# Optimization experiments

Measured on AMD Instinct MI355X. Metric: run time of the kernel, lower is better.

## Reference

```python
import jax, jax.numpy as jnp
import numpy as np

E, T, D, H = 8, 2048, 1024, 4096  # experts, tokens/expert, n_embed, n_mlp_hidden


def setup_inputs() -> dict:
    key = jax.random.key(0)
    ks = jax.random.split(key, 4)
    return {
        "x": jax.random.normal(ks[0], (E, T, D), dtype=jnp.float32),
        "w_c_fc": jax.random.normal(ks[1], (E, D, H), dtype=jnp.float32) * 0.02,
        "b_c_fc": jnp.zeros((E, 1, H), dtype=jnp.float32),
        "w_gate": jax.random.normal(ks[2], (E, D, H), dtype=jnp.float32) * 0.02,
        "b_gate": jnp.zeros((E, 1, H), dtype=jnp.float32),
        "w_c_proj": jax.random.normal(ks[3], (E, H, D), dtype=jnp.float32) * (0.02 * (2 * 12) ** -0.5),
        "b_c_proj": jnp.zeros((E, 1, D), dtype=jnp.float32),
    }


def reference(x, w_c_fc, b_c_fc, w_gate, b_gate, w_c_proj, b_c_proj):
    # Per-expert batched GEMMs with gated activation: silu(h * g)
    h = jnp.einsum('eti,eih->eth', x, w_c_fc) + b_c_fc
    g = jnp.einsum('eti,eih->eth', x, w_gate) + b_gate
    o = jnp.einsum('eth,eho->eto', jax.nn.silu(h * g), w_c_proj) + b_c_proj
    return o
```

## Files before the change

### kernel.cpp

```cpp
#include <hip/hip_runtime.h>
#include <hip/hip_bf16.h>
#include <stdint.h>


#define T_ 2048
#define D_ 1024
#define H_ 4096
#define NE 8

typedef unsigned short u16;
typedef __attribute__((ext_vector_type(8))) u16 u16x8;
typedef __attribute__((ext_vector_type(4))) u16 u16x4;
typedef __attribute__((ext_vector_type(8))) short bf16x8;
typedef __attribute__((ext_vector_type(4))) float f32x4;

__device__ __forceinline__ uint32_t bf16_rne(float f) {
    union { float f; uint32_t u; } v; v.f = f;
    return (v.u + 0x7FFFu + ((v.u >> 16) & 1u)) >> 16;
}

__device__ __forceinline__ void gload16(const void* g, void* l) {
    __builtin_amdgcn_global_load_lds((const __attribute__((address_space(1))) void*)g,
                                     (__attribute__((address_space(3))) void*)l,
                                     16, 0, 0);
}

#define SBAR() __builtin_amdgcn_s_barrier()

__global__ __launch_bounds__(256) void tobf16_kernel(const float* __restrict__ in,
    u16* __restrict__ oh, int n4) {
    int i = blockIdx.x * 256 + threadIdx.x;
    if (i >= n4) return;
    float4 v = reinterpret_cast<const float4*>(in)[i];
    float c[4] = {v.x, v.y, v.z, v.w};
    u16x4 h{};
#pragma unroll
    for (int j = 0; j < 4; ++j) h[j] = (u16)bf16_rne(c[j]);
    reinterpret_cast<u16x4*>(oh)[i] = h;
}

__global__ __launch_bounds__(256) void transpose_hi_kernel(
    const float* __restrict__ in, u16* __restrict__ oh, int R, int C) {
    __shared__ float tile[64][65];
    const int z = blockIdx.z;
    const int r0 = blockIdx.x * 64, c0 = blockIdx.y * 64;
    const float* src = in + (size_t)z * R * C;
    const int tr = threadIdx.x >> 4;
    const int tc = (threadIdx.x & 15) * 4;
#pragma unroll
    for (int j = 0; j < 4; ++j) {
        const float4 v = *reinterpret_cast<const float4*>(&src[(size_t)(r0 + tr + j*16) * C + c0 + tc]);
        tile[tr + j*16][tc+0] = v.x; tile[tr + j*16][tc+1] = v.y;
        tile[tr + j*16][tc+2] = v.z; tile[tr + j*16][tc+3] = v.w;
    }
    __syncthreads();
    const int cl = threadIdx.x & 63;
    const int q  = threadIdx.x >> 6;
    u16x8 h0{}, h1{};
#pragma unroll
    for (int rr = 0; rr < 8; ++rr) h0[rr] = (u16)bf16_rne(tile[q*16 + rr][cl]);
#pragma unroll
    for (int rr = 0; rr < 8; ++rr) h1[rr] = (u16)bf16_rne(tile[q*16 + 8 + rr][cl]);
    size_t ob = ((size_t)z * C + c0 + cl) * R + r0 + q*16;
    *reinterpret_cast<u16x8*>(&oh[ob])     = h0;
    *reinterpret_cast<u16x8*>(&oh[ob + 8]) = h1;
}


template<bool PF, bool RD, int VM>
__device__ __forceinline__ void duo_step(int tt, u16 (*sm)[16384],
    const u16* asrc, const u16* bsrc, const u16* gsrc, size_t a16str,
    int adst0, int adst1, int bdst, int gdst,
    int aoff, int boff, int goff,
    bf16x8 (&Ac)[4], bf16x8 (&Bc)[4], bf16x8 (&Gc)[4],
    bf16x8 (&An)[4], bf16x8 (&Bn)[4],
    f32x4 (&acch)[4][4], f32x4 (&accg)[4][4])
{
    if (VM == 4)      asm volatile("s_waitcnt vmcnt(4)" ::: "memory");
    else if (VM == 0) asm volatile("s_waitcnt vmcnt(0)" ::: "memory");
    SBAR();
    __builtin_amdgcn_sched_barrier(0);
    const u16* sb = &sm[tt & 3][0];
    const u16* nb = &sm[(tt + 1) & 3][0];
    u16* db = &sm[(tt + 3) & 3][0];
#pragma unroll
    for (int i = 0; i < 4; ++i) Gc[i] = *(const bf16x8*)(sb + goff + i * 512);
    if (PF) {
        gload16(asrc + (size_t)(tt + 3) * 32, db + adst0);
        gload16(asrc + (size_t)(tt + 3) * 32 + a16str, db + adst1);
    }
    __builtin_amdgcn_s_setprio(1);
#pragma unroll
    for (int mi = 0; mi < 4; ++mi)
#pragma unroll
        for (int ni = 0; ni < 4; ++ni)
            acch[mi][ni] = __builtin_amdgcn_mfma_f32_16x16x32_bf16(Ac[mi], Bc[ni], acch[mi][ni], 0, 0, 0);
    __builtin_amdgcn_s_setprio(0);
    if (RD) {
#pragma unroll
        for (int i = 0; i < 4; ++i) An[i] = *(const bf16x8*)(nb + aoff + i * 512);
#pragma unroll
        for (int i = 0; i < 4; ++i) Bn[i] = *(const bf16x8*)(nb + boff + i * 512);
    }
    if (PF) {
        gload16(bsrc + (size_t)(tt + 3) * 32, db + bdst);
        gload16(gsrc + (size_t)(tt + 3) * 32, db + gdst);
    }
    __builtin_amdgcn_s_setprio(1);
#pragma unroll
    for (int mi = 0; mi < 4; ++mi)
#pragma unroll
        for (int ni = 0; ni < 4; ++ni)
            accg[mi][ni] = __builtin_amdgcn_mfma_f32_16x16x32_bf16(Ac[mi], Gc[ni], accg[mi][ni], 0, 0, 0);
    __builtin_amdgcn_s_setprio(0);
}

__global__ __launch_bounds__(512, 2) void gemm_fc_gate(
    const u16* __restrict__ xh, const u16* __restrict__ fh, const u16* __restrict__ gh,
    const float* __restrict__ bfc, const float* __restrict__ bgt,
    u16* __restrict__ act)
{
    __shared__ __align__(16) u16 sm[4][16384];
    const int z  = blockIdx.z;
    const int lin = blockIdx.x + (blockIdx.y << 3);
    const int swz = ((lin & 7) << 5) + (lin >> 3);
    const int m0 = (swz & 7) * 256;
    const int n0 = (swz >> 3) * 128;
    const int tid = threadIdx.x;
    const int lane = tid & 63;
    const int wid = tid >> 6;
    const int wr = wid >> 1;
    const int wc = wid & 1;

    const int cs = ((lane & 3) ^ ((lane >> 3) & 3)) * 8;
    const u16* asrc = xh + ((size_t)z * T_ + m0 + wid * 32 + (lane >> 2)) * D_ + cs;
    const u16* bsrc = fh + ((size_t)z * H_ + n0 + wid * 16 + (lane >> 2)) * D_ + cs;
    const u16* gsrc = gh + ((size_t)z * H_ + n0 + wid * 16 + (lane >> 2)) * D_ + cs;
    const int adst0 = wid * 1024;
    const int adst1 = adst0 + 512;
    const int bdst  = 8192 + wid * 512;
    const int gdst  = 12288 + wid * 512;

    const int cswz = (((lane & 15) >> 1) & 3);
    const int aoff = (wr * 64 + (lane & 15)) * 32 + ((lane >> 4) ^ cswz) * 8;
    const int boff = 8192 + (wc * 64 + (lane & 15)) * 32 + ((lane >> 4) ^ cswz) * 8;
    const int goff = boff + 4096;

    f32x4 acch[4][4], accg[4][4];
#pragma unroll
    for (int i = 0; i < 4; ++i)
#pragma unroll
        for (int j = 0; j < 4; ++j) {
            acch[i][j] = (f32x4){0.f, 0.f, 0.f, 0.f};
            accg[i][j] = (f32x4){0.f, 0.f, 0.f, 0.f};
        }

#pragma unroll
    for (int u = 0; u < 3; ++u) {
        u16* db = &sm[u][0];
        gload16(asrc + u * 32, db + adst0);
        gload16(asrc + u * 32 + (size_t)16 * D_, db + adst1);
        gload16(bsrc + u * 32, db + bdst);
        gload16(gsrc + u * 32, db + gdst);
    }
    asm volatile("s_waitcnt vmcnt(8)" ::: "memory");
    SBAR();
    __builtin_amdgcn_sched_barrier(0);

    bf16x8 A0[4], B0[4], G0[4], A1[4], B1[4];
#pragma unroll
    for (int i = 0; i < 4; ++i) A0[i] = *(const bf16x8*)(&sm[0][0] + aoff + i * 512);
#pragma unroll
    for (int i = 0; i < 4; ++i) B0[i] = *(const bf16x8*)(&sm[0][0] + boff + i * 512);

    const size_t a16 = (size_t)16 * D_;
#pragma unroll 2
    for (int t = 0; t < 28; t += 2) {
        duo_step<true, true, 4>(t,   sm, asrc, bsrc, gsrc, a16, adst0, adst1, bdst, gdst,
                                aoff, boff, goff, A0, B0, G0, A1, B1, acch, accg);
        duo_step<true, true, 4>(t+1, sm, asrc, bsrc, gsrc, a16, adst0, adst1, bdst, gdst,
                                aoff, boff, goff, A1, B1, G0, A0, B0, acch, accg);
    }
    duo_step<true,  true,  4>(28, sm, asrc, bsrc, gsrc, a16, adst0, adst1, bdst, gdst,
                              aoff, boff, goff, A0, B0, G0, A1, B1, acch, accg);
    duo_step<false, true,  4>(29, sm, asrc, bsrc, gsrc, a16, adst0, adst1, bdst, gdst,
                              aoff, boff, goff, A1, B1, G0, A0, B0, acch, accg);
    duo_step<false, true,  0>(30, sm, asrc, bsrc, gsrc, a16, adst0, adst1, bdst, gdst,
                              aoff, boff, goff, A0, B0, G0, A1, B1, acch, accg);
    duo_step<false, false, -1>(31, sm, asrc, bsrc, gsrc, a16, adst0, adst1, bdst, gdst,
                              aoff, boff, goff, A1, B1, G0, A0, B0, acch, accg);

#pragma unroll
    for (int mi = 0; mi < 4; ++mi) {
#pragma unroll
        for (int ni = 0; ni < 4; ++ni) {
            const int col = n0 + wc * 64 + ni * 16 + (lane & 15);
            const float bh = bfc[(size_t)z * H_ + col];
            const float bg = bgt[(size_t)z * H_ + col];
#pragma unroll
            for (int r = 0; r < 4; ++r) {
                const int row = m0 + wr * 64 + mi * 16 + (lane >> 4) * 4 + r;
                float h = acch[mi][ni][r] + bh;
                float g = accg[mi][ni][r] + bg;
                float zz = h * g;
                float s = zz * __builtin_amdgcn_rcpf(1.0f + __expf(-zz));
                act[((size_t)z * T_ + row) * H_ + col] = (u16)bf16_rne(s);
            }
        }
    }
}

__global__ __launch_bounds__(512, 2) void gemm_proj(
    const u16* __restrict__ act, const u16* __restrict__ ph,
    const float* __restrict__ bp, float* __restrict__ out)
{
    __shared__ __align__(16) u16 sm[4][16384];
    const int z  = blockIdx.z;
    const int lin = blockIdx.x;
    const int m0 = (lin & 7) * 256;
    const int n0 = (lin >> 3) * 256;
    const int tid = threadIdx.x;
    const int lane = tid & 63;
    const int wid = tid >> 6;
    const int wr = wid >> 1;
    const int wc = wid & 1;

    const int cs = ((lane & 3) ^ ((lane >> 3) & 3)) * 8;
    const u16* asrc = act + ((size_t)z * T_ + m0 + wid * 32 + (lane >> 2)) * H_ + cs;
    const u16* bsrc = ph  + ((size_t)z * D_ + n0 + wid * 16 + (lane >> 2)) * H_ + cs;
    const u16* gsrc = ph  + ((size_t)z * D_ + n0 + 128 + wid * 16 + (lane >> 2)) * H_ + cs;
    const int adst0 = wid * 1024;
    const int adst1 = adst0 + 512;
    const int bdst  = 8192 + wid * 512;
    const int gdst  = 12288 + wid * 512;

    const int cswz = (((lane & 15) >> 1) & 3);
    const int aoff = (wr * 64 + (lane & 15)) * 32 + ((lane >> 4) ^ cswz) * 8;
    const int boff = 8192 + (wc * 64 + (lane & 15)) * 32 + ((lane >> 4) ^ cswz) * 8;
    const int goff = boff + 4096;

    f32x4 acch[4][4], accg[4][4];
#pragma unroll
    for (int i = 0; i < 4; ++i)
#pragma unroll
        for (int j = 0; j < 4; ++j) {
            acch[i][j] = (f32x4){0.f, 0.f, 0.f, 0.f};
            accg[i][j] = (f32x4){0.f, 0.f, 0.f, 0.f};
        }

#pragma unroll
    for (int u = 0; u < 3; ++u) {
        u16* db = &sm[u][0];
        gload16(asrc + u * 32, db + adst0);
        gload16(asrc + u * 32 + (size_t)16 * H_, db + adst1);
        gload16(bsrc + u * 32, db + bdst);
        gload16(gsrc + u * 32, db + gdst);
    }
    asm volatile("s_waitcnt vmcnt(8)" ::: "memory");
    SBAR();
    __builtin_amdgcn_sched_barrier(0);

    bf16x8 A0[4], B0[4], G0[4], A1[4], B1[4];
#pragma unroll
    for (int i = 0; i < 4; ++i) A0[i] = *(const bf16x8*)(&sm[0][0] + aoff + i * 512);
#pragma unroll
    for (int i = 0; i < 4; ++i) B0[i] = *(const bf16x8*)(&sm[0][0] + boff + i * 512);

    const size_t a16 = (size_t)16 * H_;
#pragma unroll 2
    for (int t = 0; t < 124; t += 2) {
        duo_step<true, true, 4>(t,   sm, asrc, bsrc, gsrc, a16, adst0, adst1, bdst, gdst,
                                aoff, boff, goff, A0, B0, G0, A1, B1, acch, accg);
        duo_step<true, true, 4>(t+1, sm, asrc, bsrc, gsrc, a16, adst0, adst1, bdst, gdst,
                                aoff, boff, goff, A1, B1, G0, A0, B0, acch, accg);
    }
    duo_step<true,  true,  4>(124, sm, asrc, bsrc, gsrc, a16, adst0, adst1, bdst, gdst,
                              aoff, boff, goff, A0, B0, G0, A1, B1, acch, accg);
    duo_step<false, true,  4>(125, sm, asrc, bsrc, gsrc, a16, adst0, adst1, bdst, gdst,
                              aoff, boff, goff, A1, B1, G0, A0, B0, acch, accg);
    duo_step<false, true,  0>(126, sm, asrc, bsrc, gsrc, a16, adst0, adst1, bdst, gdst,
                              aoff, boff, goff, A0, B0, G0, A1, B1, acch, accg);
    duo_step<false, false, -1>(127, sm, asrc, bsrc, gsrc, a16, adst0, adst1, bdst, gdst,
                              aoff, boff, goff, A1, B1, G0, A0, B0, acch, accg);

#pragma unroll
    for (int mi = 0; mi < 4; ++mi) {
#pragma unroll
        for (int ni = 0; ni < 4; ++ni) {
            const int colh = n0 + wc * 64 + ni * 16 + (lane & 15);
            const int colg = colh + 128;
            const float bvh = bp[(size_t)z * D_ + colh];
            const float bvg = bp[(size_t)z * D_ + colg];
#pragma unroll
            for (int r = 0; r < 4; ++r) {
                const int row = m0 + wr * 64 + mi * 16 + (lane >> 4) * 4 + r;
                out[((size_t)z * T_ + row) * D_ + colh] = acch[mi][ni][r] + bvh;
                out[((size_t)z * T_ + row) * D_ + colg] = accg[mi][ni][r] + bvg;
            }
        }
    }
}

extern "C" void kernel_launch(void* const* d_in, const int* in_sizes, int n_in,
                              void* d_out, int out_size, void* d_ws, size_t ws_size,
                              hipStream_t stream) {
    const float* x   = (const float*)d_in[0];
    const float* wfc = (const float*)d_in[1];
    const float* bfc = (const float*)d_in[2];
    const float* wg  = (const float*)d_in[3];
    const float* bg  = (const float*)d_in[4];
    const float* wp  = (const float*)d_in[5];
    const float* bp  = (const float*)d_in[6];
    float* out = (float*)d_out;

    const size_t per_e = ((size_t)T_*D_ + 3*(size_t)D_*H_ + (size_t)T_*H_) * 2;
    int EB = (int)(ws_size / per_e);
    if (EB < 1) EB = 1;
    if (EB > NE) EB = NE;

    for (int e0 = 0; e0 < NE; e0 += EB) {
        const int eb = (NE - e0 < EB) ? (NE - e0) : EB;
        char* p = (char*)d_ws;
        u16* xh = (u16*)p; p += (size_t)eb*T_*D_*2;
        u16* fh = (u16*)p; p += (size_t)eb*D_*H_*2;
        u16* gh = (u16*)p; p += (size_t)eb*D_*H_*2;
        u16* ph = (u16*)p; p += (size_t)eb*H_*D_*2;
        u16* act = (u16*)p;

        const int n4 = eb * T_ * D_ / 4;
        tobf16_kernel<<<dim3((n4 + 255) / 256), 256, 0, stream>>>(
            x + (size_t)e0*T_*D_, xh, n4);
        transpose_hi_kernel<<<dim3(D_/64, H_/64, eb), 256, 0, stream>>>(
            wfc + (size_t)e0*D_*H_, fh, D_, H_);
        transpose_hi_kernel<<<dim3(D_/64, H_/64, eb), 256, 0, stream>>>(
            wg + (size_t)e0*D_*H_, gh, D_, H_);
        transpose_hi_kernel<<<dim3(H_/64, D_/64, eb), 256, 0, stream>>>(
            wp + (size_t)e0*H_*D_, ph, H_, D_);
        gemm_fc_gate<<<dim3(8, 32, eb), 512, 0, stream>>>(
            xh, fh, gh, bfc + (size_t)e0*H_, bg + (size_t)e0*H_, act);
        gemm_proj<<<dim3(32, 1, eb), 512, 0, stream>>>(
            act, ph, bp + (size_t)e0*D_, out + (size_t)e0*T_*D_);
    }
}
```

Measured before the change: 582.0 us.

## Halve waves per block, double per-wave M tile with interleaved MFMA/LDS schedule

Both GEMM kernels move from 512 to 256 threads per block, so each wave now computes a 128x64 tile (8x4 MFMA fragments for both accumulators) and issues twice the global->LDS loads. The step function is rewritten to interleave eight MFMA groups with LDS fragment reads for the next stage and global prefetches, separated by sched_barriers, and the G fragments are now double-buffered too. The aim is higher MFMA density per wave and better overlap of memory traffic with compute, at the cost of much higher register pressure (launch_bounds 256,1) and possibly lower occupancy or spills.

```diff
diff --git a/kernel.cpp b/kernel.cpp
--- a/kernel.cpp
+++ b/kernel.cpp
@@ -26,6 +26,7 @@
 }
 
 #define SBAR() __builtin_amdgcn_s_barrier()
+#define SB0()  __builtin_amdgcn_sched_barrier(0)
 
 __global__ __launch_bounds__(256) void tobf16_kernel(const float* __restrict__ in,
     u16* __restrict__ oh, int n4) {
@@ -67,55 +68,68 @@
 }
 
 
+#define MFMA_GRP(mi) \
+  _Pragma("unroll") for (int ni = 0; ni < 4; ++ni) \
+      acch[mi][ni] = __builtin_amdgcn_mfma_f32_16x16x32_bf16(Ac[mi], Bc[ni], acch[mi][ni], 0, 0, 0); \
+  _Pragma("unroll") for (int ni = 0; ni < 4; ++ni) \
+      accg[mi][ni] = __builtin_amdgcn_mfma_f32_16x16x32_bf16(Ac[mi], Gc[ni], accg[mi][ni], 0, 0, 0);
+
 template<bool PF, bool RD, int VM>
-__device__ __forceinline__ void duo_step(int tt, u16 (*sm)[16384],
-    const u16* asrc, const u16* bsrc, const u16* gsrc, size_t a16str,
-    int adst0, int adst1, int bdst, int gdst,
-    int aoff, int boff, int goff,
-    bf16x8 (&Ac)[4], bf16x8 (&Bc)[4], bf16x8 (&Gc)[4],
-    bf16x8 (&An)[4], bf16x8 (&Bn)[4],
-    f32x4 (&acch)[4][4], f32x4 (&accg)[4][4])
+__device__ __forceinline__ void duo4_step(int tt, u16 (*sm)[16384],
+    const u16* asrc, const u16* bsrc, const u16* gsrc, size_t lda,
+    int adst, int bdst, int gdst, int aoff, int boff, int goff,
+    bf16x8 (&Ac)[8], bf16x8 (&Bc)[4], bf16x8 (&Gc)[4],
+    bf16x8 (&An)[8], bf16x8 (&Bn)[4], bf16x8 (&Gn)[4],
+    f32x4 (&acch)[8][4], f32x4 (&accg)[8][4])
 {
-    if (VM == 4)      asm volatile("s_waitcnt vmcnt(4)" ::: "memory");
-    else if (VM == 0) asm volatile("s_waitcnt vmcnt(0)" ::: "memory");
-    SBAR();
-    __builtin_amdgcn_sched_barrier(0);
-    const u16* sb = &sm[tt & 3][0];
     const u16* nb = &sm[(tt + 1) & 3][0];
     u16* db = &sm[(tt + 3) & 3][0];
-#pragma unroll
-    for (int i = 0; i < 4; ++i) Gc[i] = *(const bf16x8*)(sb + goff + i * 512);
+    const size_t k0 = (size_t)(tt + 3) * 32;
+    if (VM == 8)      asm volatile("s_waitcnt vmcnt(8)" ::: "memory");
+    else if (VM == 0) asm volatile("s_waitcnt vmcnt(0)" ::: "memory");
+    if (VM >= 0) SBAR();
+    SB0();
+    MFMA_GRP(0); SB0();
+    if (RD) {
+#pragma unroll
+        for (int i = 0; i < 4; ++i) An[i] = *(const bf16x8*)(nb + aoff + i * 512);
+    }
+    SB0(); MFMA_GRP(1); SB0();
+    if (RD) {
+#pragma unroll
+        for (int i = 0; i < 4; ++i) An[4 + i] = *(const bf16x8*)(nb + aoff + (4 + i) * 512);
+    }
+    SB0(); MFMA_GRP(2); SB0();
+    if (RD) {
+#pragma unroll
+        for (int i = 0; i < 4; ++i) Bn[i] = *(const bf16x8*)(nb + boff + i * 512);
+    }
+    SB0(); MFMA_GRP(3); SB0();
+    if (RD) {
+#pragma unroll
+        for (int i = 0; i < 4; ++i) Gn[i] = *(const bf16x8*)(nb + goff + i * 512);
+    }
+    SB0(); MFMA_GRP(4); SB0();
     if (PF) {
-        gload16(asrc + (size_t)(tt + 3) * 32, db + adst0);
-        gload16(asrc + (size_t)(tt + 3) * 32 + a16str, db + adst1);
-    }
-    __builtin_amdgcn_s_setprio(1);
-#pragma unroll
-    for (int mi = 0; mi < 4; ++mi)
-#pragma unroll
-        for (int ni = 0; ni < 4; ++ni)
-            acch[mi][ni] = __builtin_amdgcn_mfma_f32_16x16x32_bf16(Ac[mi], Bc[ni], acch[mi][ni], 0, 0, 0);
-    __builtin_amdgcn_s_setprio(0);
-    if (RD) {
-#pragma unroll
-        for (int i = 0; i < 4; ++i) An[i] = *(const bf16x8*)(nb + aoff + i * 512);
-#pragma unroll
-        for (int i = 0; i < 4; ++i) Bn[i] = *(const bf16x8*)(nb + boff + i * 512);
-    }
+        gload16(asrc + k0,                 db + adst);
+        gload16(asrc + k0 + 16 * lda,      db + adst + 512);
+    }
+    SB0(); MFMA_GRP(5); SB0();
     if (PF) {
-        gload16(bsrc + (size_t)(tt + 3) * 32, db + bdst);
-        gload16(gsrc + (size_t)(tt + 3) * 32, db + gdst);
-    }
-    __builtin_amdgcn_s_setprio(1);
-#pragma unroll
-    for (int mi = 0; mi < 4; ++mi)
-#pragma unroll
-        for (int ni = 0; ni < 4; ++ni)
-            accg[mi][ni] = __builtin_amdgcn_mfma_f32_16x16x32_bf16(Ac[mi], Gc[ni], accg[mi][ni], 0, 0, 0);
-    __builtin_amdgcn_s_setprio(0);
-}
-
-__global__ __launch_bounds__(512, 2) void gemm_fc_gate(
+        gload16(asrc + k0 + 32 * lda,      db + adst + 1024);
+        gload16(asrc + k0 + 48 * lda,      db + adst + 1536);
+    }
+    SB0(); MFMA_GRP(6); SB0();
+    if (PF) {
+        gload16(bsrc + k0,                 db + bdst);
+        gload16(bsrc + k0 + 16 * lda,      db + bdst + 512);
+        gload16(gsrc + k0,                 db + gdst);
+        gload16(gsrc + k0 + 16 * lda,      db + gdst + 512);
+    }
+    SB0(); MFMA_GRP(7);
+}
+
+__global__ __launch_bounds__(256, 1) void gemm_fc_gate(
     const u16* __restrict__ xh, const u16* __restrict__ fh, const u16* __restrict__ gh,
     const float* __restrict__ bfc, const float* __restrict__ bgt,
     u16* __restrict__ act)
@@ -133,22 +147,21 @@
     const int wc = wid & 1;
 
     const int cs = ((lane & 3) ^ ((lane >> 3) & 3)) * 8;
-    const u16* asrc = xh + ((size_t)z * T_ + m0 + wid * 32 + (lane >> 2)) * D_ + cs;
-    const u16* bsrc = fh + ((size_t)z * H_ + n0 + wid * 16 + (lane >> 2)) * D_ + cs;
-    const u16* gsrc = gh + ((size_t)z * H_ + n0 + wid * 16 + (lane >> 2)) * D_ + cs;
-    const int adst0 = wid * 1024;
-    const int adst1 = adst0 + 512;
-    const int bdst  = 8192 + wid * 512;
-    const int gdst  = 12288 + wid * 512;
+    const u16* asrc = xh + ((size_t)z * T_ + m0 + wid * 64 + (lane >> 2)) * D_ + cs;
+    const u16* bsrc = fh + ((size_t)z * H_ + n0 + wid * 32 + (lane >> 2)) * D_ + cs;
+    const u16* gsrc = gh + ((size_t)z * H_ + n0 + wid * 32 + (lane >> 2)) * D_ + cs;
+    const int adst = wid * 2048;
+    const int bdst = 8192 + wid * 1024;
+    const int gdst = 12288 + wid * 1024;
 
     const int cswz = (((lane & 15) >> 1) & 3);
-    const int aoff = (wr * 64 + (lane & 15)) * 32 + ((lane >> 4) ^ cswz) * 8;
+    const int aoff = (wr * 128 + (lane & 15)) * 32 + ((lane >> 4) ^ cswz) * 8;
     const int boff = 8192 + (wc * 64 + (lane & 15)) * 32 + ((lane >> 4) ^ cswz) * 8;
     const int goff = boff + 4096;
 
-    f32x4 acch[4][4], accg[4][4];
-#pragma unroll
-    for (int i = 0; i < 4; ++i)
+    f32x4 acch[8][4], accg[8][4];
+#pragma unroll
+    for (int i = 0; i < 8; ++i)
 #pragma unroll
         for (int j = 0; j < 4; ++j) {
             acch[i][j] = (f32x4){0.f, 0.f, 0.f, 0.f};
@@ -158,40 +171,44 @@
 #pragma unroll
     for (int u = 0; u < 3; ++u) {
         u16* db = &sm[u][0];
-        gload16(asrc + u * 32, db + adst0);
-        gload16(asrc + u * 32 + (size_t)16 * D_, db + adst1);
-        gload16(bsrc + u * 32, db + bdst);
-        gload16(gsrc + u * 32, db + gdst);
-    }
-    asm volatile("s_waitcnt vmcnt(8)" ::: "memory");
+        const size_t k0 = (size_t)u * 32;
+#pragma unroll
+        for (int a = 0; a < 4; ++a)
+            gload16(asrc + k0 + (size_t)(16 * a) * D_, db + adst + a * 512);
+        gload16(bsrc + k0, db + bdst);
+        gload16(bsrc + k0 + (size_t)16 * D_, db + bdst + 512);
+        gload16(gsrc + k0, db + gdst);
+        gload16(gsrc + k0 + (size_t)16 * D_, db + gdst + 512);
+    }
+    asm volatile("s_waitcnt vmcnt(16)" ::: "memory");
     SBAR();
-    __builtin_amdgcn_sched_barrier(0);
-
-    bf16x8 A0[4], B0[4], G0[4], A1[4], B1[4];
-#pragma unroll
-    for (int i = 0; i < 4; ++i) A0[i] = *(const bf16x8*)(&sm[0][0] + aoff + i * 512);
+    SB0();
+
+    bf16x8 A0[8], B0[4], G0[4], A1[8], B1[4], G1[4];
+#pragma unroll
+    for (int i = 0; i < 8; ++i) A0[i] = *(const bf16x8*)(&sm[0][0] + aoff + i * 512);
 #pragma unroll
     for (int i = 0; i < 4; ++i) B0[i] = *(const bf16x8*)(&sm[0][0] + boff + i * 512);
-
-    const size_t a16 = (size_t)16 * D_;
-#pragma unroll 2
+#pragma unroll
+    for (int i = 0; i < 4; ++i) G0[i] = *(const bf16x8*)(&sm[0][0] + goff + i * 512);
+
     for (int t = 0; t < 28; t += 2) {
-        duo_step<true, true, 4>(t,   sm, asrc, bsrc, gsrc, a16, adst0, adst1, bdst, gdst,
-                                aoff, boff, goff, A0, B0, G0, A1, B1, acch, accg);
-        duo_step<true, true, 4>(t+1, sm, asrc, bsrc, gsrc, a16, adst0, adst1, bdst, gdst,
-                                aoff, boff, goff, A1, B1, G0, A0, B0, acch, accg);
-    }
-    duo_step<true,  true,  4>(28, sm, asrc, bsrc, gsrc, a16, adst0, adst1, bdst, gdst,
-                              aoff, boff, goff, A0, B0, G0, A1, B1, acch, accg);
-    duo_step<false, true,  4>(29, sm, asrc, bsrc, gsrc, a16, adst0, adst1, bdst, gdst,
-                              aoff, boff, goff, A1, B1, G0, A0, B0, acch, accg);
-    duo_step<false, true,  0>(30, sm, asrc, bsrc, gsrc, a16, adst0, adst1, bdst, gdst,
-                              aoff, boff, goff, A0, B0, G0, A1, B1, acch, accg);
-    duo_step<false, false, -1>(31, sm, asrc, bsrc, gsrc, a16, adst0, adst1, bdst, gdst,
-                              aoff, boff, goff, A1, B1, G0, A0, B0, acch, accg);
-
-#pragma unroll
-    for (int mi = 0; mi < 4; ++mi) {
+        duo4_step<true, true, 8>(t,   sm, asrc, bsrc, gsrc, D_, adst, bdst, gdst,
+                                 aoff, boff, goff, A0, B0, G0, A1, B1, G1, acch, accg);
+        duo4_step<true, true, 8>(t+1, sm, asrc, bsrc, gsrc, D_, adst, bdst, gdst,
+                                 aoff, boff, goff, A1, B1, G1, A0, B0, G0, acch, accg);
+    }
+    duo4_step<true,  true,  8>(28, sm, asrc, bsrc, gsrc, D_, adst, bdst, gdst,
+                               aoff, boff, goff, A0, B0, G0, A1, B1, G1, acch, accg);
+    duo4_step<false, true,  8>(29, sm, asrc, bsrc, gsrc, D_, adst, bdst, gdst,
+                               aoff, boff, goff, A1, B1, G1, A0, B0, G0, acch, accg);
+    duo4_step<false, true,  0>(30, sm, asrc, bsrc, gsrc, D_, adst, bdst, gdst,
+                               aoff, boff, goff, A0, B0, G0, A1, B1, G1, acch, accg);
+    duo4_step<false, false, -1>(31, sm, asrc, bsrc, gsrc, D_, adst, bdst, gdst,
+                               aoff, boff, goff, A1, B1, G1, A0, B0, G0, acch, accg);
+
+#pragma unroll
+    for (int mi = 0; mi < 8; ++mi) {
 #pragma unroll
         for (int ni = 0; ni < 4; ++ni) {
             const int col = n0 + wc * 64 + ni * 16 + (lane & 15);
@@ -199,7 +216,7 @@
             const float bg = bgt[(size_t)z * H_ + col];
 #pragma unroll
             for (int r = 0; r < 4; ++r) {
-                const int row = m0 + wr * 64 + mi * 16 + (lane >> 4) * 4 + r;
+                const int row = m0 + wr * 128 + mi * 16 + (lane >> 4) * 4 + r;
                 float h = acch[mi][ni][r] + bh;
                 float g = accg[mi][ni][r] + bg;
                 float zz = h * g;
@@ -210,7 +227,7 @@
     }
 }
 
-__global__ __launch_bounds__(512, 2) void gemm_proj(
+__global__ __launch_bounds__(256, 1) void gemm_proj(
     const u16* __restrict__ act, const u16* __restrict__ ph,
     const float* __restrict__ bp, float* __restrict__ out)
 {
@@ -226,22 +243,21 @@
     const int wc = wid & 1;
 
     const int cs = ((lane & 3) ^ ((lane >> 3) & 3)) * 8;
-    const u16* asrc = act + ((size_t)z * T_ + m0 + wid * 32 + (lane >> 2)) * H_ + cs;
-    const u16* bsrc = ph  + ((size_t)z * D_ + n0 + wid * 16 + (lane >> 2)) * H_ + cs;
-    const u16* gsrc = ph  + ((size_t)z * D_ + n0 + 128 + wid * 16 + (lane >> 2)) * H_ + cs;
-    const int adst0 = wid * 1024;
-    const int adst1 = adst0 + 512;
-    const int bdst  = 8192 + wid * 512;
-    const int gdst  = 12288 + wid * 512;
+    const u16* asrc = act + ((size_t)z * T_ + m0 + wid * 64 + (lane >> 2)) * H_ + cs;
+    const u16* bsrc = ph  + ((size_t)z * D_ + n0 + wid * 32 + (lane >> 2)) * H_ + cs;
+    const u16* gsrc = ph  + ((size_t)z * D_ + n0 + 128 + wid * 32 + (lane >> 2)) * H_ + cs;
+    const int adst = wid * 2048;
+    const int bdst = 8192 + wid * 1024;
+    const int gdst = 12288 + wid * 1024;
 
     const int cswz = (((lane & 15) >> 1) & 3);
-    const int aoff = (wr * 64 + (lane & 15)) * 32 + ((lane >> 4) ^ cswz) * 8;
+    const int aoff = (wr * 128 + (lane & 15)) * 32 + ((lane >> 4) ^ cswz) * 8;
     const int boff = 8192 + (wc * 64 + (lane & 15)) * 32 + ((lane >> 4) ^ cswz) * 8;
     const int goff = boff + 4096;
 
-    f32x4 acch[4][4], accg[4][4];
-#pragma unroll
-    for (int i = 0; i < 4; ++i)
+    f32x4 acch[8][4], accg[8][4];
+#pragma unroll
+    for (int i = 0; i < 8; ++i)
 #pragma unroll
         for (int j = 0; j < 4; ++j) {
             acch[i][j] = (f32x4){0.f, 0.f, 0.f, 0.f};
@@ -251,40 +267,44 @@
 #pragma unroll
     for (int u = 0; u < 3; ++u) {
         u16* db = &sm[u][0];
-        gload16(asrc + u * 32, db + adst0);
-        gload16(asrc + u * 32 + (size_t)16 * H_, db + adst1);
-        gload16(bsrc + u * 32, db + bdst);
-        gload16(gsrc + u * 32, db + gdst);
-    }
-    asm volatile("s_waitcnt vmcnt(8)" ::: "memory");
+        const size_t k0 = (size_t)u * 32;
+#pragma unroll
+        for (int a = 0; a < 4; ++a)
+            gload16(asrc + k0 + (size_t)(16 * a) * H_, db + adst + a * 512);
+        gload16(bsrc + k0, db + bdst);
+        gload16(bsrc + k0 + (size_t)16 * H_, db + bdst + 512);
+        gload16(gsrc + k0, db + gdst);
+        gload16(gsrc + k0 + (size_t)16 * H_, db + gdst + 512);
+    }
+    asm volatile("s_waitcnt vmcnt(16)" ::: "memory");
     SBAR();
-    __builtin_amdgcn_sched_barrier(0);
-
-    bf16x8 A0[4], B0[4], G0[4], A1[4], B1[4];
-#pragma unroll
-    for (int i = 0; i < 4; ++i) A0[i] = *(const bf16x8*)(&sm[0][0] + aoff + i * 512);
+    SB0();
+
+    bf16x8 A0[8], B0[4], G0[4], A1[8], B1[4], G1[4];
+#pragma unroll
+    for (int i = 0; i < 8; ++i) A0[i] = *(const bf16x8*)(&sm[0][0] + aoff + i * 512);
 #pragma unroll
     for (int i = 0; i < 4; ++i) B0[i] = *(const bf16x8*)(&sm[0][0] + boff + i * 512);
-
-    const size_t a16 = (size_t)16 * H_;
-#pragma unroll 2
+#pragma unroll
+    for (int i = 0; i < 4; ++i) G0[i] = *(const bf16x8*)(&sm[0][0] + goff + i * 512);
+
     for (int t = 0; t < 124; t += 2) {
-        duo_step<true, true, 4>(t,   sm, asrc, bsrc, gsrc, a16, adst0, adst1, bdst, gdst,
-                                aoff, boff, goff, A0, B0, G0, A1, B1, acch, accg);
-        duo_step<true, true, 4>(t+1, sm, asrc, bsrc, gsrc, a16, adst0, adst1, bdst, gdst,
-                                aoff, boff, goff, A1, B1, G0, A0, B0, acch, accg);
-    }
-    duo_step<true,  true,  4>(124, sm, asrc, bsrc, gsrc, a16, adst0, adst1, bdst, gdst,
-                              aoff, boff, goff, A0, B0, G0, A1, B1, acch, accg);
-    duo_step<false, true,  4>(125, sm, asrc, bsrc, gsrc, a16, adst0, adst1, bdst, gdst,
-                              aoff, boff, goff, A1, B1, G0, A0, B0, acch, accg);
-    duo_step<false, true,  0>(126, sm, asrc, bsrc, gsrc, a16, adst0, adst1, bdst, gdst,
-                              aoff, boff, goff, A0, B0, G0, A1, B1, acch, accg);
-    duo_step<false, false, -1>(127, sm, asrc, bsrc, gsrc, a16, adst0, adst1, bdst, gdst,
-                              aoff, boff, goff, A1, B1, G0, A0, B0, acch, accg);
-
-#pragma unroll
-    for (int mi = 0; mi < 4; ++mi) {
+        duo4_step<true, true, 8>(t,   sm, asrc, bsrc, gsrc, H_, adst, bdst, gdst,
+                                 aoff, boff, goff, A0, B0, G0, A1, B1, G1, acch, accg);
+        duo4_step<true, true, 8>(t+1, sm, asrc, bsrc, gsrc, H_, adst, bdst, gdst,
+                                 aoff, boff, goff, A1, B1, G1, A0, B0, G0, acch, accg);
+    }
+    duo4_step<true,  true,  8>(124, sm, asrc, bsrc, gsrc, H_, adst, bdst, gdst,
+                               aoff, boff, goff, A0, B0, G0, A1, B1, G1, acch, accg);
+    duo4_step<false, true,  8>(125, sm, asrc, bsrc, gsrc, H_, adst, bdst, gdst,
+                               aoff, boff, goff, A1, B1, G1, A0, B0, G0, acch, accg);
+    duo4_step<false, true,  0>(126, sm, asrc, bsrc, gsrc, H_, adst, bdst, gdst,
+                               aoff, boff, goff, A0, B0, G0, A1, B1, G1, acch, accg);
+    duo4_step<false, false, -1>(127, sm, asrc, bsrc, gsrc, H_, adst, bdst, gdst,
+                               aoff, boff, goff, A1, B1, G1, A0, B0, G0, acch, accg);
+
+#pragma unroll
+    for (int mi = 0; mi < 8; ++mi) {
 #pragma unroll
         for (int ni = 0; ni < 4; ++ni) {
             const int colh = n0 + wc * 64 + ni * 16 + (lane & 15);
@@ -293,7 +313,7 @@
             const float bvg = bp[(size_t)z * D_ + colg];
 #pragma unroll
             for (int r = 0; r < 4; ++r) {
-                const int row = m0 + wr * 64 + mi * 16 + (lane >> 4) * 4 + r;
+                const int row = m0 + wr * 128 + mi * 16 + (lane >> 4) * 4 + r;
                 out[((size_t)z * T_ + row) * D_ + colh] = acch[mi][ni][r] + bvh;
                 out[((size_t)z * T_ + row) * D_ + colg] = accg[mi][ni][r] + bvg;
             }
@@ -336,9 +356,9 @@
             wg + (size_t)e0*D_*H_, gh, D_, H_);
         transpose_hi_kernel<<<dim3(H_/64, D_/64, eb), 256, 0, stream>>>(
             wp + (size_t)e0*H_*D_, ph, H_, D_);
-        gemm_fc_gate<<<dim3(8, 32, eb), 512, 0, stream>>>(
+        gemm_fc_gate<<<dim3(8, 32, eb), 256, 0, stream>>>(
             xh, fh, gh, bfc + (size_t)e0*H_, bg + (size_t)e0*H_, act);
-        gemm_proj<<<dim3(32, 1, eb), 512, 0, stream>>>(
+        gemm_proj<<<dim3(32, 1, eb), 256, 0, stream>>>(
             act, ph, bp + (size_t)e0*D_, out + (size_t)e0*T_*D_);
     }
 }
```

Measured after the change: 623.9 us. 1.07x slower.
